# Kernel tuning notes

Hardware: AMD Instinct MI355X
Metric: run time of the kernel (lower is better)

## Reference

```python
import jax, jax.numpy as jnp
import numpy as np

# ---- dims (match init_kwargs / input_specs) ----
B, T_H, NR = 32, 128, 1      # batch, rollout horizon t, n_ref (= n_x = n_y)
L, D, H = 6, 128, 4          # n_layer, n_embd, n_head
T = T_H + 1                  # GPT sequence buffer length (U has t+1 entries)
DH = D // H
STD = 0.02


def setup_inputs() -> dict:
    key = jax.random.key(0)
    ks = jax.random.split(key, 16)
    p = {}
    p["data"] = jax.random.uniform(ks[0], (B, 2), jnp.float32)          # plant params p0, p1
    p["r"] = jax.random.normal(ks[1], (B, T_H, NR), jnp.float32)        # reference signal
    # GPT params
    p["wte_w"] = jax.random.normal(ks[2], (2 * NR, D), jnp.float32) * STD
    p["wte_b"] = jnp.zeros((D,), jnp.float32)
    p["wpe"] = jax.random.normal(ks[3], (T, D), jnp.float32) * STD
    p["ln1_w"] = jnp.ones((L, D), jnp.float32)
    p["ln1_b"] = jnp.zeros((L, D), jnp.float32)
    p["ln2_w"] = jnp.ones((L, D), jnp.float32)
    p["ln2_b"] = jnp.zeros((L, D), jnp.float32)
    p["qkv_w"] = jax.random.normal(ks[4], (L, D, 3 * D), jnp.float32) * STD
    p["qkv_b"] = jnp.zeros((L, 3 * D), jnp.float32)
    p["attn_proj_w"] = jax.random.normal(ks[5], (L, D, D), jnp.float32) * STD
    p["attn_proj_b"] = jnp.zeros((L, D), jnp.float32)
    p["fc_w"] = jax.random.normal(ks[6], (L, D, 4 * D), jnp.float32) * STD
    p["fc_b"] = jnp.zeros((L, 4 * D), jnp.float32)
    p["fc2_w"] = jax.random.normal(ks[7], (L, 4 * D, D), jnp.float32) * STD
    p["fc2_b"] = jnp.zeros((L, D), jnp.float32)
    p["lnf_w"] = jnp.ones((D,), jnp.float32)
    p["lnf_b"] = jnp.zeros((D,), jnp.float32)
    p["head_w"] = jax.random.normal(ks[8], (D, NR), jnp.float32) * STD
    p["head_b"] = jnp.zeros((NR,), jnp.float32)
    return p


def _ln(x, w, b):
    m = jnp.mean(x, axis=-1, keepdims=True)
    v = jnp.var(x, axis=-1, keepdims=True)
    return (x - m) * jax.lax.rsqrt(v + 1e-5) * w + b


def reference(data, r, wte_w, wte_b, wpe, ln1_w, ln1_b, ln2_w, ln2_b,
              qkv_w, qkv_b, attn_proj_w, attn_proj_b, fc_w, fc_b,
              fc2_w, fc2_b, lnf_w, lnf_b, head_w, head_b):
    causal = jnp.tril(jnp.ones((T, T), bool))
    scale = 1.0 / np.sqrt(DH)

    def gpt(E, U):
        # E, U: [B, T, NR] zero-padded buffers; causal attention makes pos i
        # depend only on filled positions 0..i (identical to prefix forward).
        x = jnp.concatenate([E, U], axis=-1) @ wte_w + wte_b + wpe[None]  # [B,T,D]
        for l in range(L):
            h = _ln(x, ln1_w[l], ln1_b[l])
            qkv = h @ qkv_w[l] + qkv_b[l]
            q, k, v = jnp.split(qkv, 3, axis=-1)
            q = q.reshape(B, T, H, DH)
            k = k.reshape(B, T, H, DH)
            v = v.reshape(B, T, H, DH)
            att = jnp.einsum('bqhd,bkhd->bhqk', q, k) * scale
            att = jnp.where(causal[None, None], att, -1e9)
            att = jax.nn.softmax(att, axis=-1)
            o = jnp.einsum('bhqk,bkhd->bqhd', att, v).reshape(B, T, D)
            x = x + o @ attn_proj_w[l] + attn_proj_b[l]
            h2 = _ln(x, ln2_w[l], ln2_b[l])
            x = x + jax.nn.gelu(h2 @ fc_w[l] + fc_b[l]) @ fc2_w[l] + fc2_b[l]
        x = _ln(x, lnf_w, lnf_b)
        return x @ head_w + head_b  # [B, T, NR]

    p0 = data[:, 0:1]  # [B,1]
    p1 = data[:, 1:2]

    def step(carry, i):
        E, U, Y, s = carry          # s == y_i == x_i (nx == ny)
        e_i = jnp.take(r, i, axis=1) - s       # [B, NR]
        Y = Y.at[:, i].set(s)
        E = E.at[:, i].set(e_i)
        pred = gpt(E, U)
        u_next = jnp.take(pred, i, axis=1)     # last valid position == i
        U = U.at[:, i + 1].set(u_next)
        # ODE plant: Euler step with Ts = 1
        z = p0 * s                               # intermediate_vars
        x_dot = -z + p1 * jnp.tanh(u_next)       # dynamics
        s_next = s + 1.0 * x_dot
        return (E, U, Y, s_next), None

    E0 = jnp.zeros((B, T, NR), jnp.float32)
    U0 = jnp.zeros((B, T, NR), jnp.float32)    # U[:, 0] = 0
    Y0 = jnp.zeros((B, T_H, NR), jnp.float32)
    s0 = jnp.zeros((B, NR), jnp.float32)
    (E, U, Y, s), _ = jax.lax.scan(step, (E0, U0, Y0, s0), jnp.arange(T_H))
    return Y
```

## Files before the change

kernel.cpp:

```cpp
#include <hip/hip_runtime.h>
#include <math.h>

#define NB   32
#define TH   128
#define NL   6
#define DD   128
#define NH   4
#define DHD  32
#define TCAP 128
#define D3   384
#define D4   512

typedef _Float16 f16;
typedef _Float16 f16x8 __attribute__((ext_vector_type(8)));

__global__ void prep_kernel(const float* __restrict__ qkv, const float* __restrict__ proj,
                            const float* __restrict__ fc,  const float* __restrict__ fc2,
                            f16* __restrict__ out) {
    int i = blockIdx.x * blockDim.x + threadIdx.x;
    const int n0 = NL * DD * D3, n1 = NL * DD * DD, n2 = NL * DD * D4, n3 = NL * D4 * DD;
    const int total = n0 + n1 + n2 + n3;
    if (i >= total) return;
    float v;
    if (i < n0)                 v = qkv[i];
    else if (i < n0 + n1)       v = proj[i - n0];
    else if (i < n0 + n1 + n2)  v = fc[i - n0 - n1];
    else                        v = fc2[i - n0 - n1 - n2];
    out[i] = (f16)v;
}

template<int CTRL>
__device__ __forceinline__ float dpp_add_f(float v) {
    int t = __builtin_amdgcn_update_dpp(0, __float_as_int(v), CTRL, 0xF, 0xF, true);
    return v + __int_as_float(t);
}
template<int CTRL>
__device__ __forceinline__ float dpp_max_f(float v) {
    int iv = __float_as_int(v);
    int t = __builtin_amdgcn_update_dpp(iv, iv, CTRL, 0xF, 0xF, false);
    return fmaxf(v, __int_as_float(t));
}
__device__ __forceinline__ float wave_sum_bcast(float v) {
    v = dpp_add_f<0x111>(v);
    v = dpp_add_f<0x112>(v);
    v = dpp_add_f<0x114>(v);
    v = dpp_add_f<0x118>(v);
    v = dpp_add_f<0x142>(v);
    v = dpp_add_f<0x143>(v);
    return __int_as_float(__builtin_amdgcn_readlane(__float_as_int(v), 63));
}
__device__ __forceinline__ float wave_max_bcast(float v) {
    v = dpp_max_f<0x111>(v);
    v = dpp_max_f<0x112>(v);
    v = dpp_max_f<0x114>(v);
    v = dpp_max_f<0x118>(v);
    v = dpp_max_f<0x142>(v);
    v = dpp_max_f<0x143>(v);
    return __int_as_float(__builtin_amdgcn_readlane(__float_as_int(v), 63));
}
__device__ __forceinline__ float red8_16_32(float v) {
    v = dpp_add_f<0x108>(v);
    v += __shfl_xor(v, 16);
    v += __shfl_xor(v, 32);
    return v;
}
__device__ __forceinline__ float red4_32(float v) {
    v = dpp_add_f<0x104>(v);
    v = dpp_add_f<0x108>(v);
    v += __shfl_xor(v, 16);
    v += __shfl_xor(v, 32);
    return v;
}
__device__ __forceinline__ float red2_32(float v) {
    v = dpp_add_f<0x102>(v);
    v = dpp_add_f<0x104>(v);
    v = dpp_add_f<0x108>(v);
    v += __shfl_xor(v, 16);
    v += __shfl_xor(v, 32);
    return v;
}

__device__ __forceinline__ float gelu_tanh(float v) {
    float t = v * v * v;
    return 0.5f * v * (1.f + tanhf(0.7978845608028654f * (v + 0.044715f * t)));
}

__device__ __forceinline__ void bar_lds() {
    asm volatile("s_waitcnt lgkmcnt(0)" ::: "memory");
    __builtin_amdgcn_s_barrier();
    asm volatile("" ::: "memory");
}
__device__ __forceinline__ void bar_step() {
    asm volatile("s_waitcnt vmcnt(0) lgkmcnt(0)" ::: "memory");
    __builtin_amdgcn_s_barrier();
    asm volatile("" ::: "memory");
}

__global__ __launch_bounds__(512, 1) void gpt_loop(
    const float* __restrict__ data,  const float* __restrict__ r,
    const float* __restrict__ wte_w, const float* __restrict__ wte_b,
    const float* __restrict__ wpe,
    const float* __restrict__ ln1_w, const float* __restrict__ ln1_b,
    const float* __restrict__ ln2_w, const float* __restrict__ ln2_b,
    const float* __restrict__ qkv_b, const float* __restrict__ proj_b,
    const float* __restrict__ fc_b,  const float* __restrict__ fc2_b,
    const float* __restrict__ lnf_w, const float* __restrict__ lnf_b,
    const float* __restrict__ head_w,const float* __restrict__ head_b,
    const f16* __restrict__ Wq, const f16* __restrict__ Wp,
    const f16* __restrict__ Wf, const f16* __restrict__ Wf2,
    f16* __restrict__ Kc, f16* __restrict__ Vc,
    float* __restrict__ Y)
{
    const int b    = blockIdx.x;
    const int tid  = threadIdx.x;
    const int lane = tid & 63;
    const int wid  = tid >> 6;

    __shared__ __align__(16) float x[DD], qv[DD], o[DD], hmid[D4];
    __shared__ __align__(16) float sc[NH][TCAP];
    __shared__ __align__(16) f16 kvK[DD], kvV[DD];
    __shared__ __align__(16) float c_ln1w[NL][DD], c_ln1b[NL][DD], c_ln2w[NL][DD], c_ln2b[NL][DD];
    __shared__ __align__(16) float c_qkvb[NL][D3], c_projb[NL][DD], c_fcb[NL][D4], c_fc2b[NL][DD];
    __shared__ __align__(16) float c_lnfw[DD], c_lnfb[DD], c_headw[DD], c_wte0[DD], c_wte1[DD], c_wteb[DD];

    const float p0 = data[b * 2 + 0];
    const float p1 = data[b * 2 + 1];
    const float hb = head_b[0];

    f16* Kb = Kc + (size_t)b * NL * TCAP * DD;
    f16* Vb = Vc + (size_t)b * NL * TCAP * DD;

    for (int idx = tid; idx < NL * DD; idx += 512) {
        int l = idx / DD, d = idx % DD;
        c_ln1w[l][d] = ln1_w[idx]; c_ln1b[l][d] = ln1_b[idx];
        c_ln2w[l][d] = ln2_w[idx]; c_ln2b[l][d] = ln2_b[idx];
        c_projb[l][d] = proj_b[idx]; c_fc2b[l][d] = fc2_b[idx];
    }
    for (int idx = tid; idx < NL * D3; idx += 512) c_qkvb[idx / D3][idx % D3] = qkv_b[idx];
    for (int idx = tid; idx < NL * D4; idx += 512) c_fcb[idx / D4][idx % D4] = fc_b[idx];
    if (tid < DD) {
        c_lnfw[tid] = lnf_w[tid]; c_lnfb[tid] = lnf_b[tid]; c_headw[tid] = head_w[tid];
        c_wte0[tid] = wte_w[tid]; c_wte1[tid] = wte_w[DD + tid]; c_wteb[tid] = wte_b[tid];
    }
    {
        float4 z4 = make_float4(0.f, 0.f, 0.f, 0.f);
        float4* K4 = (float4*)Kb; float4* V4 = (float4*)Vb;
        const int n4 = NL * TCAP * DD * 2 / 16;
        for (int idx = tid; idx < n4; idx += 512) { K4[idx] = z4; V4[idx] = z4; }
    }
    __syncthreads();

    float s_reg = 0.f;
    if (wid == 0) {
        float e0 = r[b * TH + 0];
        x[lane]      = e0 * c_wte0[lane]      + c_wteb[lane]      + wpe[lane];
        x[lane + 64] = e0 * c_wte0[lane + 64] + c_wteb[lane + 64] + wpe[64 + lane];
    }

    const int cgq = lane & 7, ksq = lane >> 3;
    const int cbq = wid * 64 + cgq * 8, k0q = ksq * 16;
    const int cg2 = lane & 1, ks2 = lane >> 1;
    const int cb2 = (wid * 2 + cg2) * 8;
    const int hh  = wid - 4;
    const int vcg = lane & 3, vjs = lane >> 2;

    f16x8 wq[16];
    if (wid < 6) {
        const f16* W = Wq + cbq;
        #pragma unroll
        for (int k = 0; k < 16; k++) wq[k] = *(const f16x8*)(W + (size_t)(k0q + k) * D3);
    }
    __syncthreads();

    for (int i = 0; i < TH; i++) {
        const int inext = (i + 1 < TH) ? (i + 1) : (TH - 1);
        float r_next = r[b * TH + inext];
        float wpe_a  = wpe[(i + 1) * DD + lane];
        float wpe_b  = wpe[(i + 1) * DD + 64 + lane];

        for (int l = 0; l < NL; l++) {
            f16* Krow = Kb + ((size_t)l * TCAP + i) * DD;
            f16* Vrow = Vb + ((size_t)l * TCAP + i) * DD;
            const f16* Kl = Kb + (size_t)l * TCAP * DD;
            const f16* Vl = Vb + (size_t)l * TCAP * DD;

            f16x8 wp4[4];
            f16x8 wfh1[8], wfh2[8];
            f16x8 wf2h1[8], wf2h2[8];

            if (wid < 6) {
                float v0 = x[lane], v1 = x[lane + 64];
                float sm = wave_sum_bcast(v0 + v1);
                float sq = wave_sum_bcast(v0 * v0 + v1 * v1);
                float m  = sm * (1.f / DD);
                float rs = rsqrtf(sq * (1.f / DD) - m * m + 1e-5f);
                float hk[16];
                #pragma unroll
                for (int t = 0; t < 4; t++) {
                    float4 xx = *(const float4*)&x[k0q + 4 * t];
                    float4 ww = *(const float4*)&c_ln1w[l][k0q + 4 * t];
                    float4 bb = *(const float4*)&c_ln1b[l][k0q + 4 * t];
                    hk[4 * t + 0] = (xx.x - m) * rs * ww.x + bb.x;
                    hk[4 * t + 1] = (xx.y - m) * rs * ww.y + bb.y;
                    hk[4 * t + 2] = (xx.z - m) * rs * ww.z + bb.z;
                    hk[4 * t + 3] = (xx.w - m) * rs * ww.w + bb.w;
                }
                float acc[8] = {0.f,0.f,0.f,0.f,0.f,0.f,0.f,0.f};
                #pragma unroll
                for (int k = 0; k < 16; k++) {
                    f16x8 w = wq[k];
                    float hkk = hk[k];
                    #pragma unroll
                    for (int j = 0; j < 8; j++) acc[j] += hkk * (float)w[j];
                }
                #pragma unroll
                for (int j = 0; j < 8; j++) acc[j] = red8_16_32(acc[j]);
                if (ksq == 0) {
                    if (cbq < DD) {
                        #pragma unroll
                        for (int j = 0; j < 8; j++) qv[cbq + j] = acc[j] + c_qkvb[l][cbq + j];
                    } else if (cbq < 2 * DD) {
                        f16x8 kv;
                        #pragma unroll
                        for (int j = 0; j < 8; j++) kv[j] = (f16)(acc[j] + c_qkvb[l][cbq + j]);
                        *(f16x8*)(Krow + (cbq - DD)) = kv;
                        *(f16x8*)(&kvK[cbq - DD])   = kv;
                    } else {
                        f16x8 vv;
                        #pragma unroll
                        for (int j = 0; j < 8; j++) vv[j] = (f16)(acc[j] + c_qkvb[l][cbq + j]);
                        *(f16x8*)(Vrow + (cbq - 2 * DD)) = vv;
                        *(f16x8*)(&kvV[cbq - 2 * DD])   = vv;
                    }
                }
            }
            {
                const f16* W = Wp + (size_t)l * DD * DD + cb2;
                #pragma unroll
                for (int k = 0; k < 4; k++) wp4[k] = *(const f16x8*)(W + (size_t)(ks2 * 4 + k) * DD);
            }
            bar_lds();

            if (wid >= 4) {
                const int im1 = (i > 0) ? (i - 1) : 0;
                const int j0 = (lane < i) ? lane : im1;
                const int j1 = (lane + 64 < i) ? (lane + 64) : im1;
                const f16* K0p = Kl + (size_t)j0 * DD + hh * DHD;
                const f16* K1p = Kl + (size_t)j1 * DD + hh * DHD;
                f16x8 kr0[4], kr1[4], kfr[4];
                #pragma unroll
                for (int g = 0; g < 4; g++) {
                    kr0[g] = *(const f16x8*)(K0p + g * 8);
                    kr1[g] = *(const f16x8*)(K1p + g * 8);
                }
                f16x8 vreg[8];
                const f16* Vp = Vl + hh * DHD + vcg * 8;
                #pragma unroll
                for (int t = 0; t < 8; t++) {
                    int row = vjs * 8 + t; row = (row < i) ? row : im1;
                    vreg[t] = *(const f16x8*)(Vp + (size_t)row * DD);
                }
                #pragma unroll
                for (int g = 0; g < 4; g++) kfr[g] = *(const f16x8*)(&kvK[hh * DHD + g * 8]);
                f16x8 vi = *(const f16x8*)(&kvV[hh * DHD + vcg * 8]);

                const bool ok0 = (lane <= i), ok1 = (lane + 64 <= i);
                float d0 = 0.f, d1 = 0.f;
                #pragma unroll
                for (int g = 0; g < 4; g++) {
                    f16x8 ka  = (lane      >= i) ? kfr[g] : kr0[g];
                    f16x8 kb2 = (lane + 64 >= i) ? kfr[g] : kr1[g];
                    float4 qa = *(const float4*)&qv[hh * DHD + g * 8];
                    float4 qb = *(const float4*)&qv[hh * DHD + g * 8 + 4];
                    d0 += qa.x*(float)ka[0] + qa.y*(float)ka[1] + qa.z*(float)ka[2] + qa.w*(float)ka[3]
                        + qb.x*(float)ka[4] + qb.y*(float)ka[5] + qb.z*(float)ka[6] + qb.w*(float)ka[7];
                    d1 += qa.x*(float)kb2[0] + qa.y*(float)kb2[1] + qa.z*(float)kb2[2] + qa.w*(float)kb2[3]
                        + qb.x*(float)kb2[4] + qb.y*(float)kb2[5] + qb.z*(float)kb2[6] + qb.w*(float)kb2[7];
                }
                const float sscale = 0.17677669529663687f;
                float s0 = ok0 ? d0 * sscale : -1e30f;
                float s1 = ok1 ? d1 * sscale : -1e30f;
                float mx = wave_max_bcast(fmaxf(s0, s1));
                float e0 = ok0 ? expf(s0 - mx) : 0.f;
                float e1 = ok1 ? expf(s1 - mx) : 0.f;
                float inv = 1.f / wave_sum_bcast(e0 + e1);
                sc[hh][lane]      = e0 * inv;
                sc[hh][lane + 64] = e1 * inv;
                __builtin_amdgcn_wave_barrier();
                const int ja = vjs * 8;
                float4 pa = *(const float4*)&sc[hh][ja];
                float4 pb = *(const float4*)&sc[hh][ja + 4];
                float pv[8] = {pa.x, pa.y, pa.z, pa.w, pb.x, pb.y, pb.z, pb.w};
                float a[8] = {0.f,0.f,0.f,0.f,0.f,0.f,0.f,0.f};
                #pragma unroll
                for (int t = 0; t < 8; t++) {
                    f16x8 vv = (ja + t == i) ? vi : vreg[t];
                    float p = pv[t];
                    #pragma unroll
                    for (int u = 0; u < 8; u++) a[u] += p * (float)vv[u];
                }
                #pragma unroll
                for (int u = 0; u < 8; u++) a[u] = red4_32(a[u]);
                if (vjs == 0) {
                    #pragma unroll
                    for (int u = 0; u < 8; u++) o[hh * DHD + vcg * 8 + u] = a[u];
                }
            }
            {
                const f16* W2 = Wf + (size_t)l * DD * D4 + cbq;
                #pragma unroll
                for (int k = 0; k < 8; k++) wfh1[k] = *(const f16x8*)(W2 + (size_t)(k0q + k) * D4);
            }
            bar_lds();

            {
                float4 ov = *(const float4*)&o[ks2 * 4];
                float oo[4] = {ov.x, ov.y, ov.z, ov.w};
                float acc[8] = {0.f,0.f,0.f,0.f,0.f,0.f,0.f,0.f};
                #pragma unroll
                for (int k = 0; k < 4; k++) {
                    f16x8 w = wp4[k];
                    float ok_ = oo[k];
                    #pragma unroll
                    for (int j = 0; j < 8; j++) acc[j] += ok_ * (float)w[j];
                }
                {
                    const f16* W2 = Wf + (size_t)l * DD * D4 + cbq;
                    #pragma unroll
                    for (int k = 0; k < 8; k++) wfh2[k] = *(const f16x8*)(W2 + (size_t)(k0q + 8 + k) * D4);
                }
                #pragma unroll
                for (int j = 0; j < 8; j++) acc[j] = red2_32(acc[j]);
                if (ks2 == 0) {
                    #pragma unroll
                    for (int j = 0; j < 8; j++) x[cb2 + j] += acc[j] + c_projb[l][cb2 + j];
                }
            }
            bar_lds();

            {
                float v0 = x[lane], v1 = x[lane + 64];
                float sm = wave_sum_bcast(v0 + v1);
                float sq = wave_sum_bcast(v0 * v0 + v1 * v1);
                float m  = sm * (1.f / DD);
                float rs = rsqrtf(sq * (1.f / DD) - m * m + 1e-5f);
                float hk[16];
                #pragma unroll
                for (int t = 0; t < 4; t++) {
                    float4 xx = *(const float4*)&x[k0q + 4 * t];
                    float4 ww = *(const float4*)&c_ln2w[l][k0q + 4 * t];
                    float4 bb = *(const float4*)&c_ln2b[l][k0q + 4 * t];
                    hk[4 * t + 0] = (xx.x - m) * rs * ww.x + bb.x;
                    hk[4 * t + 1] = (xx.y - m) * rs * ww.y + bb.y;
                    hk[4 * t + 2] = (xx.z - m) * rs * ww.z + bb.z;
                    hk[4 * t + 3] = (xx.w - m) * rs * ww.w + bb.w;
                }
                float acc[8] = {0.f,0.f,0.f,0.f,0.f,0.f,0.f,0.f};
                #pragma unroll
                for (int k = 0; k < 8; k++) {
                    f16x8 w = wfh1[k];
                    float hkk = hk[k];
                    #pragma unroll
                    for (int j = 0; j < 8; j++) acc[j] += hkk * (float)w[j];
                }
                {
                    const f16* W = Wf2 + (size_t)l * D4 * DD + cb2;
                    #pragma unroll
                    for (int k = 0; k < 8; k++) wf2h1[k] = *(const f16x8*)(W + (size_t)(ks2 * 16 + k) * DD);
                }
                #pragma unroll
                for (int k = 0; k < 8; k++) {
                    f16x8 w = wfh2[k];
                    float hkk = hk[8 + k];
                    #pragma unroll
                    for (int j = 0; j < 8; j++) acc[j] += hkk * (float)w[j];
                }
                {
                    const f16* W = Wf2 + (size_t)l * D4 * DD + cb2;
                    #pragma unroll
                    for (int k = 0; k < 8; k++) wf2h2[k] = *(const f16x8*)(W + (size_t)(ks2 * 16 + 8 + k) * DD);
                }
                #pragma unroll
                for (int j = 0; j < 8; j++) acc[j] = red8_16_32(acc[j]);
                if (ksq == 0) {
                    #pragma unroll
                    for (int j = 0; j < 8; j++) hmid[cbq + j] = gelu_tanh(acc[j] + c_fcb[l][cbq + j]);
                }
            }
            bar_lds();

            {
                float mk[16];
                #pragma unroll
                for (int t = 0; t < 4; t++) {
                    float4 mm = *(const float4*)&hmid[ks2 * 16 + 4 * t];
                    mk[4 * t + 0] = mm.x; mk[4 * t + 1] = mm.y;
                    mk[4 * t + 2] = mm.z; mk[4 * t + 3] = mm.w;
                }
                const int ln = (l + 1 == NL) ? 0 : (l + 1);
                float acc[8] = {0.f,0.f,0.f,0.f,0.f,0.f,0.f,0.f};
                #pragma unroll
                for (int k = 0; k < 8; k++) {
                    f16x8 w = wf2h1[k];
                    float mkk = mk[k];
                    #pragma unroll
                    for (int j = 0; j < 8; j++) acc[j] += mkk * (float)w[j];
                }
                if (wid < 6) {
                    const f16* W = Wq + (size_t)ln * DD * D3 + cbq;
                    #pragma unroll
                    for (int k = 0; k < 8; k++) wq[k] = *(const f16x8*)(W + (size_t)(k0q + k) * D3);
                }
                #pragma unroll
                for (int k = 0; k < 8; k++) {
                    f16x8 w = wf2h2[k];
                    float mkk = mk[8 + k];
                    #pragma unroll
                    for (int j = 0; j < 8; j++) acc[j] += mkk * (float)w[j];
                }
                if (wid < 6) {
                    const f16* W = Wq + (size_t)ln * DD * D3 + cbq;
                    #pragma unroll
                    for (int k = 0; k < 8; k++) wq[8 + k] = *(const f16x8*)(W + (size_t)(k0q + 8 + k) * D3);
                }
                #pragma unroll
                for (int j = 0; j < 8; j++) acc[j] = red2_32(acc[j]);
                if (ks2 == 0) {
                    #pragma unroll
                    for (int j = 0; j < 8; j++) x[cb2 + j] += acc[j] + c_fc2b[l][cb2 + j];
                }
            }
            bar_lds();
        }

        if (wid == 0) {
            float v0 = x[lane], v1 = x[lane + 64];
            float sm = wave_sum_bcast(v0 + v1);
            float sq = wave_sum_bcast(v0 * v0 + v1 * v1);
            float m  = sm * (1.f / DD);
            float rs = rsqrtf(sq * (1.f / DD) - m * m + 1e-5f);
            float h0 = (v0 - m) * rs * c_lnfw[lane]      + c_lnfb[lane];
            float h1 = (v1 - m) * rs * c_lnfw[lane + 64] + c_lnfb[lane + 64];
            float v  = wave_sum_bcast(h0 * c_headw[lane] + h1 * c_headw[lane + 64]);
            float un = v + hb;
            float s  = s_reg;
            if (lane == 0) Y[b * TH + i] = s;
            float sn = s + (-p0 * s + p1 * tanhf(un));
            s_reg = sn;
            float e = r_next - sn;
            x[lane]      = e * c_wte0[lane]      + un * c_wte1[lane]      + c_wteb[lane]      + wpe_a;
            x[lane + 64] = e * c_wte0[lane + 64] + un * c_wte1[lane + 64] + c_wteb[lane + 64] + wpe_b;
        }
        bar_step();
    }
}

extern "C" void kernel_launch(void* const* d_in, const int* in_sizes, int n_in,
                              void* d_out, int out_size, void* d_ws, size_t ws_size,
                              hipStream_t stream) {
    const float* data   = (const float*)d_in[0];
    const float* r      = (const float*)d_in[1];
    const float* wte_w  = (const float*)d_in[2];
    const float* wte_b  = (const float*)d_in[3];
    const float* wpe    = (const float*)d_in[4];
    const float* ln1_w  = (const float*)d_in[5];
    const float* ln1_b  = (const float*)d_in[6];
    const float* ln2_w  = (const float*)d_in[7];
    const float* ln2_b  = (const float*)d_in[8];
    const float* qkv_w  = (const float*)d_in[9];
    const float* qkv_b  = (const float*)d_in[10];
    const float* proj_w = (const float*)d_in[11];
    const float* proj_b = (const float*)d_in[12];
    const float* fc_w   = (const float*)d_in[13];
    const float* fc_b   = (const float*)d_in[14];
    const float* fc2_w  = (const float*)d_in[15];
    const float* fc2_b  = (const float*)d_in[16];
    const float* lnf_w  = (const float*)d_in[17];
    const float* lnf_b  = (const float*)d_in[18];
    const float* head_w = (const float*)d_in[19];
    const float* head_b = (const float*)d_in[20];

    f16* wsp = (f16*)d_ws;
    f16* Wq  = wsp;
    f16* Wp  = Wq  + NL * DD * D3;
    f16* Wf  = Wp  + NL * DD * DD;
    f16* Wf2 = Wf  + NL * DD * D4;
    f16* Kc  = Wf2 + NL * D4 * DD;
    f16* Vc  = Kc  + (size_t)NB * NL * TCAP * DD;

    const int n_w = NL * DD * D3 + NL * DD * DD + NL * DD * D4 + NL * D4 * DD;
    prep_kernel<<<(n_w + 255) / 256, 256, 0, stream>>>(qkv_w, proj_w, fc_w, fc2_w, Wq);

    gpt_loop<<<NB, 512, 0, stream>>>(
        data, r, wte_w, wte_b, wpe, ln1_w, ln1_b, ln2_w, ln2_b,
        qkv_b, proj_b, fc_b, fc2_b, lnf_w, lnf_b, head_w, head_b,
        Wq, Wp, Wf, Wf2, Kc, Vc, (float*)d_out);
}
```

Before: 7.675 ms.

## Fuse attention-proj and FC2 into producer waves with LDS atomics, cutting barriers

Each attention wave (4-7) now computes its own head's slice of the output projection and atomically adds it into the residual in LDS. Each of the 8 waves computes the FC2 partial for its own 64-wide hidden slice and atomically accumulates into a double-buffered residual. This removes two block-wide barriers per layer and replaces cross-wave gathers with intra-wave barriers. It adds LDS float atomics, which make the summation order nondeterministic, and it changes register pressure through the transposed weight prefetch layouts.

```diff
diff --git a/kernel.cpp b/kernel.cpp
--- a/kernel.cpp
+++ b/kernel.cpp
@@ -12,6 +12,7 @@
 #define D4   512
 
 typedef _Float16 f16;
+typedef _Float16 f16x4 __attribute__((ext_vector_type(4)));
 typedef _Float16 f16x8 __attribute__((ext_vector_type(8)));
 
 __global__ void prep_kernel(const float* __restrict__ qkv, const float* __restrict__ proj,
@@ -41,21 +42,15 @@
     return fmaxf(v, __int_as_float(t));
 }
 __device__ __forceinline__ float wave_sum_bcast(float v) {
-    v = dpp_add_f<0x111>(v);
-    v = dpp_add_f<0x112>(v);
-    v = dpp_add_f<0x114>(v);
-    v = dpp_add_f<0x118>(v);
-    v = dpp_add_f<0x142>(v);
-    v = dpp_add_f<0x143>(v);
+    v = dpp_add_f<0x111>(v); v = dpp_add_f<0x112>(v);
+    v = dpp_add_f<0x114>(v); v = dpp_add_f<0x118>(v);
+    v = dpp_add_f<0x142>(v); v = dpp_add_f<0x143>(v);
     return __int_as_float(__builtin_amdgcn_readlane(__float_as_int(v), 63));
 }
 __device__ __forceinline__ float wave_max_bcast(float v) {
-    v = dpp_max_f<0x111>(v);
-    v = dpp_max_f<0x112>(v);
-    v = dpp_max_f<0x114>(v);
-    v = dpp_max_f<0x118>(v);
-    v = dpp_max_f<0x142>(v);
-    v = dpp_max_f<0x143>(v);
+    v = dpp_max_f<0x111>(v); v = dpp_max_f<0x112>(v);
+    v = dpp_max_f<0x114>(v); v = dpp_max_f<0x118>(v);
+    v = dpp_max_f<0x142>(v); v = dpp_max_f<0x143>(v);
     return __int_as_float(__builtin_amdgcn_readlane(__float_as_int(v), 63));
 }
 __device__ __forceinline__ float red8_16_32(float v) {
@@ -65,14 +60,6 @@
     return v;
 }
 __device__ __forceinline__ float red4_32(float v) {
-    v = dpp_add_f<0x104>(v);
-    v = dpp_add_f<0x108>(v);
-    v += __shfl_xor(v, 16);
-    v += __shfl_xor(v, 32);
-    return v;
-}
-__device__ __forceinline__ float red2_32(float v) {
-    v = dpp_add_f<0x102>(v);
     v = dpp_add_f<0x104>(v);
     v = dpp_add_f<0x108>(v);
     v += __shfl_xor(v, 16);
@@ -116,7 +103,8 @@
     const int lane = tid & 63;
     const int wid  = tid >> 6;
 
-    __shared__ __align__(16) float x[DD], qv[DD], o[DD], hmid[D4];
+    __shared__ __align__(16) float xb[2][DD];
+    __shared__ __align__(16) float qv[DD], o[DD], hmid[D4];
     __shared__ __align__(16) float sc[NH][TCAP];
     __shared__ __align__(16) f16 kvK[DD], kvV[DD];
     __shared__ __align__(16) float c_ln1w[NL][DD], c_ln1b[NL][DD], c_ln2w[NL][DD], c_ln2b[NL][DD];
@@ -153,16 +141,16 @@
     float s_reg = 0.f;
     if (wid == 0) {
         float e0 = r[b * TH + 0];
-        x[lane]      = e0 * c_wte0[lane]      + c_wteb[lane]      + wpe[lane];
-        x[lane + 64] = e0 * c_wte0[lane + 64] + c_wteb[lane + 64] + wpe[64 + lane];
+        xb[0][lane]      = e0 * c_wte0[lane]      + c_wteb[lane]      + wpe[lane];
+        xb[0][lane + 64] = e0 * c_wte0[lane + 64] + c_wteb[lane + 64] + wpe[64 + lane];
     }
 
     const int cgq = lane & 7, ksq = lane >> 3;
     const int cbq = wid * 64 + cgq * 8, k0q = ksq * 16;
-    const int cg2 = lane & 1, ks2 = lane >> 1;
-    const int cb2 = (wid * 2 + cg2) * 8;
     const int hh  = wid - 4;
     const int vcg = lane & 3, vjs = lane >> 2;
+    const int pcg = lane & 31, pks = lane >> 5;
+    const int fcg = lane & 15, fks = lane >> 4;
 
     f16x8 wq[16];
     if (wid < 6) {
@@ -179,17 +167,18 @@
         float wpe_b  = wpe[(i + 1) * DD + 64 + lane];
 
         for (int l = 0; l < NL; l++) {
+            const int pl = l & 1;
+            float* xcur = xb[pl];
+            float* xnxt = xb[1 - pl];
             f16* Krow = Kb + ((size_t)l * TCAP + i) * DD;
             f16* Vrow = Vb + ((size_t)l * TCAP + i) * DD;
             const f16* Kl = Kb + (size_t)l * TCAP * DD;
             const f16* Vl = Vb + (size_t)l * TCAP * DD;
 
-            f16x8 wp4[4];
-            f16x8 wfh1[8], wfh2[8];
-            f16x8 wf2h1[8], wf2h2[8];
-
-            if (wid < 6) {
-                float v0 = x[lane], v1 = x[lane + 64];
+            if (wid >= 6) {
+                xnxt[(wid - 6) * 64 + lane] = 0.f;
+            } else {
+                float v0 = xcur[lane], v1 = xcur[lane + 64];
                 float sm = wave_sum_bcast(v0 + v1);
                 float sq = wave_sum_bcast(v0 * v0 + v1 * v1);
                 float m  = sm * (1.f / DD);
@@ -197,7 +186,7 @@
                 float hk[16];
                 #pragma unroll
                 for (int t = 0; t < 4; t++) {
-                    float4 xx = *(const float4*)&x[k0q + 4 * t];
+                    float4 xx = *(const float4*)&xcur[k0q + 4 * t];
                     float4 ww = *(const float4*)&c_ln1w[l][k0q + 4 * t];
                     float4 bb = *(const float4*)&c_ln1b[l][k0q + 4 * t];
                     hk[4 * t + 0] = (xx.x - m) * rs * ww.x + bb.x;
@@ -234,42 +223,45 @@
                     }
                 }
             }
-            {
-                const f16* W = Wp + (size_t)l * DD * DD + cb2;
-                #pragma unroll
-                for (int k = 0; k < 4; k++) wp4[k] = *(const f16x8*)(W + (size_t)(ks2 * 4 + k) * DD);
+            f16x4 wpt[16];
+            if (wid >= 4) {
+                const f16* W = Wp + (size_t)l * DD * DD + (size_t)(hh * DHD + pks * 16) * DD + pcg * 4;
+                #pragma unroll
+                for (int k = 0; k < 16; k++) wpt[k] = *(const f16x4*)(W + (size_t)k * DD);
             }
             bar_lds();
 
-            if (wid >= 4) {
+            f16x8 wfh1[8], wfh2[8];
+            if (wid < 4) {
+                const f16* W2 = Wf + (size_t)l * DD * D4 + cbq;
+                #pragma unroll
+                for (int k = 0; k < 8; k++) wfh1[k] = *(const f16x8*)(W2 + (size_t)(k0q + k) * D4);
+                #pragma unroll
+                for (int k = 0; k < 8; k++) wfh2[k] = *(const f16x8*)(W2 + (size_t)(k0q + 8 + k) * D4);
+            } else {
                 const int im1 = (i > 0) ? (i - 1) : 0;
                 const int j0 = (lane < i) ? lane : im1;
                 const int j1 = (lane + 64 < i) ? (lane + 64) : im1;
                 const f16* K0p = Kl + (size_t)j0 * DD + hh * DHD;
                 const f16* K1p = Kl + (size_t)j1 * DD + hh * DHD;
-                f16x8 kr0[4], kr1[4], kfr[4];
+                f16x8 kr0[4], kr1[4];
                 #pragma unroll
                 for (int g = 0; g < 4; g++) {
                     kr0[g] = *(const f16x8*)(K0p + g * 8);
                     kr1[g] = *(const f16x8*)(K1p + g * 8);
                 }
-                f16x8 vreg[8];
-                const f16* Vp = Vl + hh * DHD + vcg * 8;
-                #pragma unroll
-                for (int t = 0; t < 8; t++) {
-                    int row = vjs * 8 + t; row = (row < i) ? row : im1;
-                    vreg[t] = *(const f16x8*)(Vp + (size_t)row * DD);
-                }
-                #pragma unroll
-                for (int g = 0; g < 4; g++) kfr[g] = *(const f16x8*)(&kvK[hh * DHD + g * 8]);
-                f16x8 vi = *(const f16x8*)(&kvV[hh * DHD + vcg * 8]);
-
-                const bool ok0 = (lane <= i), ok1 = (lane + 64 <= i);
+                if (lane == i) {
+                    #pragma unroll
+                    for (int g = 0; g < 4; g++) kr0[g] = *(const f16x8*)(&kvK[hh * DHD + g * 8]);
+                }
+                if (lane + 64 == i) {
+                    #pragma unroll
+                    for (int g = 0; g < 4; g++) kr1[g] = *(const f16x8*)(&kvK[hh * DHD + g * 8]);
+                }
                 float d0 = 0.f, d1 = 0.f;
                 #pragma unroll
                 for (int g = 0; g < 4; g++) {
-                    f16x8 ka  = (lane      >= i) ? kfr[g] : kr0[g];
-                    f16x8 kb2 = (lane + 64 >= i) ? kfr[g] : kr1[g];
+                    f16x8 ka = kr0[g], kb2 = kr1[g];
                     float4 qa = *(const float4*)&qv[hh * DHD + g * 8];
                     float4 qb = *(const float4*)&qv[hh * DHD + g * 8 + 4];
                     d0 += qa.x*(float)ka[0] + qa.y*(float)ka[1] + qa.z*(float)ka[2] + qa.w*(float)ka[3]
@@ -277,7 +269,19 @@
                     d1 += qa.x*(float)kb2[0] + qa.y*(float)kb2[1] + qa.z*(float)kb2[2] + qa.w*(float)kb2[3]
                         + qb.x*(float)kb2[4] + qb.y*(float)kb2[5] + qb.z*(float)kb2[6] + qb.w*(float)kb2[7];
                 }
+                f16x8 vreg[8];
+                const f16* Vp = Vl + hh * DHD + vcg * 8;
+                #pragma unroll
+                for (int t = 0; t < 8; t++) {
+                    int row = vjs * 8 + t; row = (row < i) ? row : im1;
+                    vreg[t] = *(const f16x8*)(Vp + (size_t)row * DD);
+                }
+                #pragma unroll
+                for (int t = 0; t < 8; t++) {
+                    if (vjs * 8 + t == i) vreg[t] = *(const f16x8*)(&kvV[hh * DHD + vcg * 8]);
+                }
                 const float sscale = 0.17677669529663687f;
+                const bool ok0 = (lane <= i), ok1 = (lane + 64 <= i);
                 float s0 = ok0 ? d0 * sscale : -1e30f;
                 float s1 = ok1 ? d1 * sscale : -1e30f;
                 float mx = wave_max_bcast(fmaxf(s0, s1));
@@ -294,7 +298,7 @@
                 float a[8] = {0.f,0.f,0.f,0.f,0.f,0.f,0.f,0.f};
                 #pragma unroll
                 for (int t = 0; t < 8; t++) {
-                    f16x8 vv = (ja + t == i) ? vi : vreg[t];
+                    f16x8 vv = vreg[t];
                     float p = pv[t];
                     #pragma unroll
                     for (int u = 0; u < 8; u++) a[u] += p * (float)vv[u];
@@ -305,41 +309,40 @@
                     #pragma unroll
                     for (int u = 0; u < 8; u++) o[hh * DHD + vcg * 8 + u] = a[u];
                 }
-            }
-            {
+                __builtin_amdgcn_wave_barrier();
+                float ov[16];
+                #pragma unroll
+                for (int t = 0; t < 4; t++) {
+                    float4 q4 = *(const float4*)&o[hh * DHD + pks * 16 + 4 * t];
+                    ov[4 * t + 0] = q4.x; ov[4 * t + 1] = q4.y;
+                    ov[4 * t + 2] = q4.z; ov[4 * t + 3] = q4.w;
+                }
+                float ap[4] = {0.f,0.f,0.f,0.f};
+                #pragma unroll
+                for (int k = 0; k < 16; k++) {
+                    f16x4 w = wpt[k];
+                    float okk = ov[k];
+                    #pragma unroll
+                    for (int j = 0; j < 4; j++) ap[j] += okk * (float)w[j];
+                }
+                #pragma unroll
+                for (int j = 0; j < 4; j++) ap[j] += __shfl_xor(ap[j], 32);
+                if (pks == 0) {
+                    #pragma unroll
+                    for (int j = 0; j < 4; j++)
+                        atomicAdd(&xcur[pcg * 4 + j],
+                                  ap[j] + (hh == 0 ? c_projb[l][pcg * 4 + j] : 0.f));
+                }
                 const f16* W2 = Wf + (size_t)l * DD * D4 + cbq;
                 #pragma unroll
                 for (int k = 0; k < 8; k++) wfh1[k] = *(const f16x8*)(W2 + (size_t)(k0q + k) * D4);
+                #pragma unroll
+                for (int k = 0; k < 8; k++) wfh2[k] = *(const f16x8*)(W2 + (size_t)(k0q + 8 + k) * D4);
             }
             bar_lds();
 
             {
-                float4 ov = *(const float4*)&o[ks2 * 4];
-                float oo[4] = {ov.x, ov.y, ov.z, ov.w};
-                float acc[8] = {0.f,0.f,0.f,0.f,0.f,0.f,0.f,0.f};
-                #pragma unroll
-                for (int k = 0; k < 4; k++) {
-                    f16x8 w = wp4[k];
-                    float ok_ = oo[k];
-                    #pragma unroll
-                    for (int j = 0; j < 8; j++) acc[j] += ok_ * (float)w[j];
-                }
-                {
-                    const f16* W2 = Wf + (size_t)l * DD * D4 + cbq;
-                    #pragma unroll
-                    for (int k = 0; k < 8; k++) wfh2[k] = *(const f16x8*)(W2 + (size_t)(k0q + 8 + k) * D4);
-                }
-                #pragma unroll
-                for (int j = 0; j < 8; j++) acc[j] = red2_32(acc[j]);
-                if (ks2 == 0) {
-                    #pragma unroll
-                    for (int j = 0; j < 8; j++) x[cb2 + j] += acc[j] + c_projb[l][cb2 + j];
-                }
-            }
-            bar_lds();
-
-            {
-                float v0 = x[lane], v1 = x[lane + 64];
+                float v0 = xcur[lane], v1 = xcur[lane + 64];
                 float sm = wave_sum_bcast(v0 + v1);
                 float sq = wave_sum_bcast(v0 * v0 + v1 * v1);
                 float m  = sm * (1.f / DD);
@@ -347,7 +350,7 @@
                 float hk[16];
                 #pragma unroll
                 for (int t = 0; t < 4; t++) {
-                    float4 xx = *(const float4*)&x[k0q + 4 * t];
+                    float4 xx = *(const float4*)&xcur[k0q + 4 * t];
                     float4 ww = *(const float4*)&c_ln2w[l][k0q + 4 * t];
                     float4 bb = *(const float4*)&c_ln2b[l][k0q + 4 * t];
                     hk[4 * t + 0] = (xx.x - m) * rs * ww.x + bb.x;
@@ -363,11 +366,6 @@
                     #pragma unroll
                     for (int j = 0; j < 8; j++) acc[j] += hkk * (float)w[j];
                 }
-                {
-                    const f16* W = Wf2 + (size_t)l * D4 * DD + cb2;
-                    #pragma unroll
-                    for (int k = 0; k < 8; k++) wf2h1[k] = *(const f16x8*)(W + (size_t)(ks2 * 16 + k) * DD);
-                }
                 #pragma unroll
                 for (int k = 0; k < 8; k++) {
                     f16x8 w = wfh2[k];
@@ -375,10 +373,11 @@
                     #pragma unroll
                     for (int j = 0; j < 8; j++) acc[j] += hkk * (float)w[j];
                 }
+                f16x8 wf2t[16];
                 {
-                    const f16* W = Wf2 + (size_t)l * D4 * DD + cb2;
-                    #pragma unroll
-                    for (int k = 0; k < 8; k++) wf2h2[k] = *(const f16x8*)(W + (size_t)(ks2 * 16 + 8 + k) * DD);
+                    const f16* W3 = Wf2 + (size_t)l * D4 * DD + (size_t)(wid * 64 + fks * 16) * DD + fcg * 8;
+                    #pragma unroll
+                    for (int k = 0; k < 16; k++) wf2t[k] = *(const f16x8*)(W3 + (size_t)k * DD);
                 }
                 #pragma unroll
                 for (int j = 0; j < 8; j++) acc[j] = red8_16_32(acc[j]);
@@ -386,55 +385,47 @@
                     #pragma unroll
                     for (int j = 0; j < 8; j++) hmid[cbq + j] = gelu_tanh(acc[j] + c_fcb[l][cbq + j]);
                 }
-            }
-            bar_lds();
-
-            {
-                float mk[16];
+                __builtin_amdgcn_wave_barrier();
+                float hv[16];
                 #pragma unroll
                 for (int t = 0; t < 4; t++) {
-                    float4 mm = *(const float4*)&hmid[ks2 * 16 + 4 * t];
-                    mk[4 * t + 0] = mm.x; mk[4 * t + 1] = mm.y;
-                    mk[4 * t + 2] = mm.z; mk[4 * t + 3] = mm.w;
-                }
-                const int ln = (l + 1 == NL) ? 0 : (l + 1);
-                float acc[8] = {0.f,0.f,0.f,0.f,0.f,0.f,0.f,0.f};
-                #pragma unroll
-                for (int k = 0; k < 8; k++) {
-                    f16x8 w = wf2h1[k];
-                    float mkk = mk[k];
-                    #pragma unroll
-                    for (int j = 0; j < 8; j++) acc[j] += mkk * (float)w[j];
-                }
-                if (wid < 6) {
-                    const f16* W = Wq + (size_t)ln * DD * D3 + cbq;
-                    #pragma unroll
-                    for (int k = 0; k < 8; k++) wq[k] = *(const f16x8*)(W + (size_t)(k0q + k) * D3);
-                }
-                #pragma unroll
-                for (int k = 0; k < 8; k++) {
-                    f16x8 w = wf2h2[k];
-                    float mkk = mk[8 + k];
-                    #pragma unroll
-                    for (int j = 0; j < 8; j++) acc[j] += mkk * (float)w[j];
-                }
-                if (wid < 6) {
-                    const f16* W = Wq + (size_t)ln * DD * D3 + cbq;
-                    #pragma unroll
-                    for (int k = 0; k < 8; k++) wq[8 + k] = *(const f16x8*)(W + (size_t)(k0q + 8 + k) * D3);
-                }
-                #pragma unroll
-                for (int j = 0; j < 8; j++) acc[j] = red2_32(acc[j]);
-                if (ks2 == 0) {
-                    #pragma unroll
-                    for (int j = 0; j < 8; j++) x[cb2 + j] += acc[j] + c_fc2b[l][cb2 + j];
+                    float4 m4 = *(const float4*)&hmid[wid * 64 + fks * 16 + 4 * t];
+                    hv[4 * t + 0] = m4.x; hv[4 * t + 1] = m4.y;
+                    hv[4 * t + 2] = m4.z; hv[4 * t + 3] = m4.w;
+                }
+                float a2[8] = {0.f,0.f,0.f,0.f,0.f,0.f,0.f,0.f};
+                #pragma unroll
+                for (int k = 0; k < 16; k++) {
+                    f16x8 w = wf2t[k];
+                    float hkk = hv[k];
+                    #pragma unroll
+                    for (int j = 0; j < 8; j++) a2[j] += hkk * (float)w[j];
+                }
+                {
+                    const int ln = (l + 1 == NL) ? 0 : (l + 1);
+                    if (wid < 6) {
+                        const f16* W = Wq + (size_t)ln * DD * D3 + cbq;
+                        #pragma unroll
+                        for (int k = 0; k < 16; k++) wq[k] = *(const f16x8*)(W + (size_t)(k0q + k) * D3);
+                    }
+                }
+                #pragma unroll
+                for (int j = 0; j < 8; j++) {
+                    a2[j] += __shfl_xor(a2[j], 16);
+                    a2[j] += __shfl_xor(a2[j], 32);
+                }
+                if (fks == 0) {
+                    #pragma unroll
+                    for (int j = 0; j < 8; j++)
+                        atomicAdd(&xnxt[fcg * 8 + j],
+                                  a2[j] + (wid == 0 ? xcur[fcg * 8 + j] + c_fc2b[l][fcg * 8 + j] : 0.f));
                 }
             }
             bar_lds();
         }
 
         if (wid == 0) {
-            float v0 = x[lane], v1 = x[lane + 64];
+            float v0 = xb[0][lane], v1 = xb[0][lane + 64];
             float sm = wave_sum_bcast(v0 + v1);
             float sq = wave_sum_bcast(v0 * v0 + v1 * v1);
             float m  = sm * (1.f / DD);
@@ -448,8 +439,8 @@
             float sn = s + (-p0 * s + p1 * tanhf(un));
             s_reg = sn;
             float e = r_next - sn;
-            x[lane]      = e * c_wte0[lane]      + un * c_wte1[lane]      + c_wteb[lane]      + wpe_a;
-            x[lane + 64] = e * c_wte0[lane + 64] + un * c_wte1[lane + 64] + c_wteb[lane + 64] + wpe_b;
+            xb[0][lane]      = e * c_wte0[lane]      + un * c_wte1[lane]      + c_wteb[lane]      + wpe_a;
+            xb[0][lane + 64] = e * c_wte0[lane + 64] + un * c_wte1[lane + 64] + c_wteb[lane + 64] + wpe_b;
         }
         bar_step();
     }
```

Result: faster. 7.343 ms (-4.3%).
